# Performance work log

Hardware: AMD Instinct MI355X
Metric: run time of the kernel (lower is better)

The kernel has to match this reference:

```python
import jax, jax.numpy as jnp
import numpy as np

DIM = 1024
NUM_HEADS = 16
HEAD_DIM = DIM // NUM_HEADS
SCALE = HEAD_DIM ** -0.5


def setup_inputs() -> dict:
    key = jax.random.key(0)
    ks = jax.random.split(key, 6)
    B, N, C = 2, 2048, DIM
    std = C ** -0.5
    return {
        "x_t": jax.random.normal(ks[0], (B, N, C), dtype=jnp.float32),
        "x_s": jax.random.normal(ks[1], (B, N, C), dtype=jnp.float32),
        "W_q": jax.random.normal(ks[2], (C, C), dtype=jnp.float32) * std,
        "W_kv": jax.random.normal(ks[3], (C, 2 * C), dtype=jnp.float32) * std,
        "W_fuse": jax.random.normal(ks[4], (C, C), dtype=jnp.float32) * std,
        "b_fuse": jax.random.normal(ks[5], (C,), dtype=jnp.float32) * 0.01,
    }


def reference(x_t, x_s, W_q, W_kv, W_fuse, b_fuse):
    B, N, C = x_t.shape
    H, D = NUM_HEADS, HEAD_DIM
    # q projection (no bias, qkv_bias=False): [B,N,C] -> [B,H,N,D]
    q = (x_t @ W_q).reshape(B, N, H, D).transpose(0, 2, 1, 3)
    # kv projection: [B,N,2C] -> k,v each [B,H,N,D]
    kv = (x_s @ W_kv).reshape(B, N, 2, H, D).transpose(2, 0, 3, 1, 4)
    k, v = kv[0], kv[1]
    # attention scores [B,H,N,N]
    attn = jnp.einsum("bhnd,bhmd->bhnm", q, k) * SCALE
    attn = jax.nn.softmax(attn, axis=-1)
    # weighted values -> [B,N,C]
    a = jnp.einsum("bhnm,bhmd->bhnd", attn, v).transpose(0, 2, 1, 3).reshape(B, N, C)
    # fuse projection (with bias); dropouts are identity (p=0)
    return a @ W_fuse + b_fuse
```

## Files before the change

kernel.cpp:

```cpp
#include <hip/hip_runtime.h>

#define SEQ 2048

typedef short short8 __attribute__((ext_vector_type(8)));
typedef float floatx4 __attribute__((ext_vector_type(4)));
typedef unsigned int uint2v __attribute__((ext_vector_type(2)));
typedef unsigned int uint4v __attribute__((ext_vector_type(4)));
typedef __fp16 f16x8 __attribute__((ext_vector_type(8)));

static __device__ __forceinline__ unsigned short f2bf(float f) {
    unsigned int u = __builtin_bit_cast(unsigned int, f);
    u = (u + 0x7fffu + ((u >> 16) & 1u)) >> 16;
    return (unsigned short)u;
}

#if __has_builtin(__builtin_amdgcn_cvt_pk_bf16_f32)
typedef __bf16 bf16x2 __attribute__((ext_vector_type(2)));
static __device__ __forceinline__ unsigned int pk_bf16(float a, float b) {
    bf16x2 v = __builtin_amdgcn_cvt_pk_bf16_f32(a, b);
    return __builtin_bit_cast(unsigned int, v);
}
#else
static __device__ __forceinline__ unsigned int pk_bf16(float a, float b) {
    return (unsigned int)f2bf(a) | ((unsigned int)f2bf(b) << 16);
}
#endif

static __device__ __forceinline__ unsigned int pk_f16(float a, float b) {
    auto v = __builtin_amdgcn_cvt_pkrtz(a, b);
    return __builtin_bit_cast(unsigned int, v);
}

#define GLD16(gp, lp)                                                        \
    __builtin_amdgcn_global_load_lds(                                        \
        (const __attribute__((address_space(1))) unsigned int*)(gp),         \
        (__attribute__((address_space(3))) unsigned int*)(lp), 16, 0, 0)

__global__ void prep_kernel(const float4* __restrict__ xa, const float4* __restrict__ xb,
                            ushort4* __restrict__ oa, ushort4* __restrict__ ob, float sa,
                            const float* __restrict__ Wq, const float* __restrict__ Wkv,
                            const float* __restrict__ Wf,
                            unsigned short* __restrict__ oq, unsigned short* __restrict__ okv,
                            unsigned short* __restrict__ of_) {
    __shared__ float tile[32][33];
    int bx = blockIdx.x, tid = threadIdx.x;
    if (bx < 8192) {
        int i = bx * 256 + tid;
        if (i < 1048576) {
            float4 v = xa[i];
            ushort4 o;
            o.x = f2bf(v.x * sa); o.y = f2bf(v.y * sa);
            o.z = f2bf(v.z * sa); o.w = f2bf(v.w * sa);
            oa[i] = o;
        } else {
            int j = i - 1048576;
            float4 v = xb[j];
            ushort4 o;
            o.x = f2bf(v.x); o.y = f2bf(v.y);
            o.z = f2bf(v.z); o.w = f2bf(v.w);
            ob[j] = o;
        }
        return;
    }
    int t2 = bx - 8192;
    const float* in; unsigned short* out; int N, t;
    if (t2 < 1024)      { in = Wq;  out = oq;  N = 1024; t = t2; }
    else if (t2 < 3072) { in = Wkv; out = okv; N = 2048; t = t2 - 1024; }
    else                { in = Wf;  out = of_; N = 1024; t = t2 - 3072; }
    int nb = N >> 5;
    int n0 = (t % nb) * 32, k0 = (t / nb) * 32;
    int tx = tid & 31, ty = tid >> 5;
#pragma unroll
    for (int i = 0; i < 4; i++)
        tile[ty + i * 8][tx] = in[(size_t)(k0 + ty + i * 8) * N + n0 + tx];
    __syncthreads();
#pragma unroll
    for (int i = 0; i < 4; i++)
        out[(size_t)(n0 + ty + i * 8) * 1024 + k0 + tx] = f2bf(tile[tx][ty + i * 8]);
}

__global__ __launch_bounds__(256, 3)
void gemm_qkv(const unsigned short* __restrict__ xt,
              const unsigned short* __restrict__ xs,
              const unsigned short* __restrict__ wq,
              const unsigned short* __restrict__ wkv,
              unsigned short* __restrict__ q_ws,
              unsigned short* __restrict__ k_ws,
              unsigned short* __restrict__ vt_ws) {
    __shared__ __align__(16) unsigned short smem_[16384];
    auto sA = (unsigned short(*)[64])smem_;
    auto sB = (unsigned short(*)[64])(smem_ + 8192);
    int tid = threadIdx.x, wave = tid >> 6, lane = tid & 63;
    int l15 = lane & 15, quad = lane >> 4;
    int cx = blockIdx.x;
    bool isq = cx < 8, isv = cx >= 16;
    const unsigned short* A  = isq ? xt : xs;
    const unsigned short* Bt = isq ? wq : wkv;
    int C0 = (isq ? cx : cx - 8) * 128;
    int R0 = blockIdx.y * 128;
    int wr = (wave >> 1) * 64, wc = (wave & 1) * 64;
    int srow = lane >> 3, scol = (lane & 7) * 8;

    floatx4 acc[4][4];
#pragma unroll
    for (int i = 0; i < 4; i++)
#pragma unroll
        for (int j = 0; j < 4; j++) acc[i][j] = (floatx4){0.f, 0.f, 0.f, 0.f};

    for (int kt = 0; kt < 16; kt++) {
        __syncthreads();
#pragma unroll
        for (int c = 0; c < 4; c++) {
            int rb = wave * 32 + c * 8;
            GLD16(&A [(size_t)(R0 + rb + srow) * 1024 + kt * 64 + scol], &sA[rb][0]);
            GLD16(&Bt[(size_t)(C0 + rb + srow) * 1024 + kt * 64 + scol], &sB[rb][0]);
        }
        __syncthreads();
#pragma unroll
        for (int ks = 0; ks < 2; ks++) {
            short8 af[4], bf[4];
#pragma unroll
            for (int mt = 0; mt < 4; mt++)
                af[mt] = *(const short8*)&sA[wr + mt * 16 + l15][ks * 32 + quad * 8];
#pragma unroll
            for (int nt = 0; nt < 4; nt++)
                bf[nt] = *(const short8*)&sB[wc + nt * 16 + l15][ks * 32 + quad * 8];
#pragma unroll
            for (int mt = 0; mt < 4; mt++)
#pragma unroll
                for (int nt = 0; nt < 4; nt++)
                    acc[mt][nt] = __builtin_amdgcn_mfma_f32_16x16x32_bf16(af[mt], bf[nt], acc[mt][nt], 0, 0, 0);
        }
    }

    int b = R0 >> 11, n0 = R0 & 2047;
    __syncthreads();

    if (!isv) {
#pragma unroll
        for (int mt = 0; mt < 4; mt++)
#pragma unroll
            for (int nt = 0; nt < 4; nt++) {
                int col = wc + nt * 16 + l15;
#pragma unroll
                for (int r = 0; r < 4; r++)
                    smem_[(wr + mt * 16 + quad * 4 + r) * 128 + col] = f2bf(acc[mt][nt][r]);
            }
        __syncthreads();
        unsigned short* out = isq ? q_ws : k_ws;
#pragma unroll
        for (int i = 0; i < 8; i++) {
            int u = tid + i * 256;
            int row = u >> 4, colg = u & 15;
            int n = n0 + row;
            int gc = C0 + colg * 8;
            int h = gc >> 6, d0 = gc & 63;
            int dd = isq ? d0 : ((((d0 >> 3) ^ (n & 7)) << 3));
            *(uint4v*)&out[((size_t)((b * 16 + h) * 2048 + n)) * 64 + dd] =
                *(const uint4v*)&smem_[row * 128 + colg * 8];
        }
    } else {
#pragma unroll
        for (int mt = 0; mt < 4; mt++)
#pragma unroll
            for (int nt = 0; nt < 4; nt++) {
                int cc = wc + nt * 16 + l15;
                int nl4 = (wr + mt * 16 + quad * 4) >> 2;
                int sw = nl4 ^ ((cc & 3) << 1);
                uint2v pk;
                pk.x = pk_f16(acc[mt][nt][0], acc[mt][nt][1]);
                pk.y = pk_f16(acc[mt][nt][2], acc[mt][nt][3]);
                *(uint2v*)&smem_[cc * 128 + (sw << 2)] = pk;
            }
        __syncthreads();
        int cb = C0 - 1024;
#pragma unroll
        for (int i = 0; i < 8; i++) {
            int u = tid + i * 256;
            int cc = u >> 4, ng = u & 15;
            int sw0 = (2 * ng) ^ ((cc & 3) << 1);
            uint4v val = *(const uint4v*)&smem_[cc * 128 + (sw0 << 2)];
            int ccv = cb + cc, h = ccv >> 6, d = ccv & 63;
            *(uint4v*)&vt_ws[((size_t)((b * 16 + h) * 64 + d)) * 2048 + n0 + ng * 8] = val;
        }
    }
}

__global__ __launch_bounds__(256, 3)
void gemm_fuse(const unsigned short* __restrict__ A,
               const unsigned short* __restrict__ Bt,
               float* __restrict__ out, const float* __restrict__ bias) {
    __shared__ unsigned short sA[128][64];
    __shared__ unsigned short sB[64][64];
    int tid = threadIdx.x, wave = tid >> 6, lane = tid & 63;
    int l15 = lane & 15, quad = lane >> 4;
    int R0 = blockIdx.y * 128, C0 = blockIdx.x * 64;
    int wr = (wave >> 1) * 64, wc = (wave & 1) * 32;
    int srow = lane >> 3, scol = (lane & 7) * 8;

    floatx4 acc[4][2];
#pragma unroll
    for (int i = 0; i < 4; i++)
#pragma unroll
        for (int j = 0; j < 2; j++) acc[i][j] = (floatx4){0.f, 0.f, 0.f, 0.f};

    for (int kt = 0; kt < 16; kt++) {
        __syncthreads();
#pragma unroll
        for (int c = 0; c < 4; c++) {
            int rb = wave * 32 + c * 8;
            GLD16(&A[(size_t)(R0 + rb + srow) * 1024 + kt * 64 + scol], &sA[rb][0]);
        }
#pragma unroll
        for (int c = 0; c < 2; c++) {
            int rb = wave * 16 + c * 8;
            GLD16(&Bt[(size_t)(C0 + rb + srow) * 1024 + kt * 64 + scol], &sB[rb][0]);
        }
        __syncthreads();
#pragma unroll
        for (int ks = 0; ks < 2; ks++) {
            short8 af[4], bf[2];
#pragma unroll
            for (int mt = 0; mt < 4; mt++)
                af[mt] = *(const short8*)&sA[wr + mt * 16 + l15][ks * 32 + quad * 8];
#pragma unroll
            for (int nt = 0; nt < 2; nt++)
                bf[nt] = *(const short8*)&sB[wc + nt * 16 + l15][ks * 32 + quad * 8];
#pragma unroll
            for (int mt = 0; mt < 4; mt++)
#pragma unroll
                for (int nt = 0; nt < 2; nt++)
                    acc[mt][nt] = __builtin_amdgcn_mfma_f32_16x16x32_bf16(af[mt], bf[nt], acc[mt][nt], 0, 0, 0);
        }
    }

#pragma unroll
    for (int mt = 0; mt < 4; mt++) {
#pragma unroll
        for (int r = 0; r < 4; r++) {
            int row = R0 + wr + mt * 16 + quad * 4 + r;
#pragma unroll
            for (int nt = 0; nt < 2; nt++) {
                int col = C0 + wc + nt * 16 + l15;
                out[(size_t)row * 1024 + col] = acc[mt][nt][r] + bias[col];
            }
        }
    }
}

__global__ __launch_bounds__(256, 2)
void attn_kernel(const unsigned short* __restrict__ Q,
                 const unsigned short* __restrict__ K,
                 const unsigned short* __restrict__ Vt,
                 unsigned short* __restrict__ Aout) {
    __shared__ __align__(16) unsigned short smem[32768];
    __shared__ float lred[4][4][16];

    int tid = threadIdx.x, wave = tid >> 6, lane = tid & 63;
    int l15 = lane & 15, quad = lane >> 4;

    int id = blockIdx.x;
    int logical = (id & 7) * 128 + (id >> 3);
    int bh = logical >> 5, qt = logical & 31;
    int b = bh >> 4, h = bh & 15;
    int qr0 = qt * 64;

    const unsigned short* Qp = Q + (size_t)bh * SEQ * 64;
    const unsigned short* Kp = K + (size_t)bh * SEQ * 64;
    const unsigned short* Vp = Vt + (size_t)bh * 64 * SEQ;

    int srow = lane >> 3, scol = (lane & 7) * 8;
    int wk0 = wave * 16;
    int vscol = scol ^ (srow << 3);

#define STAGE(t, kb)                                                          \
    {                                                                         \
        _Pragma("unroll")                                                     \
        for (int j = 0; j < 2; j++) {                                         \
            int rb = wk0 + j * 8;                                             \
            GLD16(&Kp[(size_t)((t) * 64 + rb + srow) * 64 + scol],            \
                  &smem[(kb) + rb * 64]);                                     \
            GLD16(&Vp[(size_t)(rb + srow) * 2048 + (t) * 64 + vscol],         \
                  &smem[16384 + (kb) + rb * 64]);                             \
        }                                                                     \
    }

    short8 qf[4][2];
#pragma unroll
    for (int nt = 0; nt < 4; nt++)
#pragma unroll
        for (int ks = 0; ks < 2; ks++)
            qf[nt][ks] = *(const short8*)&Qp[(size_t)(qr0 + nt * 16 + l15) * 64 + ks * 32 + quad * 8];

    STAGE(0, 0) STAGE(1, 4096) STAGE(2, 8192) STAGE(3, 12288)

    floatx4 of[4][4];
#pragma unroll
    for (int i = 0; i < 4; i++)
#pragma unroll
        for (int j = 0; j < 4; j++) of[i][j] = (floatx4){0.f, 0.f, 0.f, 0.f};
    floatx4 of_l[4];
#pragma unroll
    for (int i = 0; i < 4; i++) of_l[i] = (floatx4){0.f, 0.f, 0.f, 0.f};

    f16x8 vones;
#pragma unroll
    for (int i = 0; i < 8; i++) vones[i] = (__fp16)1.0f;

    int krow = wk0 + l15;
    int ksw = (l15 & 7) << 3;
    int kaddr0 = krow * 64 + ((quad * 8) ^ ksw);
    int kaddr1 = krow * 64 + ((32 + quad * 8) ^ ksw);
    int vcol = (wk0 + quad * 4) ^ ksw;

    asm volatile("s_waitcnt vmcnt(0)" ::: "memory");
    __syncthreads();

    auto compute_pair = [&](int kb) {
        __builtin_amdgcn_s_setprio(1);
        uint2v pka[4], pkb[4];
        {
            short8 kf0 = *(const short8*)&smem[kb + kaddr0];
            short8 kf1 = *(const short8*)&smem[kb + kaddr1];
#pragma unroll
            for (int nt = 0; nt < 4; nt++) {
                floatx4 z = (floatx4){0.f, 0.f, 0.f, 0.f};
                floatx4 s = __builtin_amdgcn_mfma_f32_16x16x32_bf16(kf0, qf[nt][0], z, 0, 0, 0);
                s = __builtin_amdgcn_mfma_f32_16x16x32_bf16(kf1, qf[nt][1], s, 0, 0, 0);
                pka[nt].x = pk_f16(__builtin_amdgcn_exp2f(s[0]), __builtin_amdgcn_exp2f(s[1]));
                pka[nt].y = pk_f16(__builtin_amdgcn_exp2f(s[2]), __builtin_amdgcn_exp2f(s[3]));
            }
        }
        {
            short8 kf0 = *(const short8*)&smem[kb + 4096 + kaddr0];
            short8 kf1 = *(const short8*)&smem[kb + 4096 + kaddr1];
#pragma unroll
            for (int nt = 0; nt < 4; nt++) {
                floatx4 z = (floatx4){0.f, 0.f, 0.f, 0.f};
                floatx4 s = __builtin_amdgcn_mfma_f32_16x16x32_bf16(kf0, qf[nt][0], z, 0, 0, 0);
                s = __builtin_amdgcn_mfma_f32_16x16x32_bf16(kf1, qf[nt][1], s, 0, 0, 0);
                pkb[nt].x = pk_f16(__builtin_amdgcn_exp2f(s[0]), __builtin_amdgcn_exp2f(s[1]));
                pkb[nt].y = pk_f16(__builtin_amdgcn_exp2f(s[2]), __builtin_amdgcn_exp2f(s[3]));
            }
        }
#pragma unroll
        for (int dt = 0; dt < 4; dt++) {
            int vbase = 16384 + kb + (dt * 16 + l15) * 64 + vcol;
            uint2v va = *(const uint2v*)&smem[vbase];
            uint2v vb = *(const uint2v*)&smem[vbase + 4096];
            f16x8 vf = __builtin_bit_cast(f16x8, (uint4v){va.x, va.y, vb.x, vb.y});
#pragma unroll
            for (int nt = 0; nt < 4; nt++) {
                f16x8 pf = __builtin_bit_cast(f16x8, (uint4v){pka[nt].x, pka[nt].y, pkb[nt].x, pkb[nt].y});
                of[dt][nt] = __builtin_amdgcn_mfma_f32_16x16x32_f16(vf, pf, of[dt][nt], 0, 0, 0);
            }
        }
#pragma unroll
        for (int nt = 0; nt < 4; nt++) {
            f16x8 pf = __builtin_bit_cast(f16x8, (uint4v){pka[nt].x, pka[nt].y, pkb[nt].x, pkb[nt].y});
            of_l[nt] = __builtin_amdgcn_mfma_f32_16x16x32_f16(vones, pf, of_l[nt], 0, 0, 0);
        }
        __builtin_amdgcn_s_setprio(0);
    };

#pragma unroll 2
    for (int p = 0; p < 14; p++) {
        int kb = (p & 1) * 8192;
        compute_pair(kb);
        __builtin_amdgcn_sched_barrier(0);
        asm volatile("s_barrier" ::: "memory");
        STAGE(2 * p + 4, kb)
        STAGE(2 * p + 5, kb + 4096)
        asm volatile("s_waitcnt vmcnt(8)" ::: "memory");
        asm volatile("s_barrier" ::: "memory");
        __builtin_amdgcn_sched_barrier(0);
    }
    compute_pair(0);
    asm volatile("s_waitcnt vmcnt(0)" ::: "memory");
    asm volatile("s_barrier" ::: "memory");
    compute_pair(8192);
#undef STAGE

    if (quad == 0) {
#pragma unroll
        for (int nt = 0; nt < 4; nt++) lred[wave][nt][l15] = of_l[nt][0];
    }
    __syncthreads();

    float* red = (float*)smem;

#define RED_WRITE(C, DTC)                                                          \
    _Pragma("unroll")                                                              \
    for (int nt = 0; nt < 4; nt++)                                                 \
        *(floatx4*)&red[((C) * 4 + wave) * 1024 + nt * 256 + lane * 4] = of[DTC][nt];

#define RED_STORE(DT, C, W0, W1, W2)                                               \
    {                                                                              \
        size_t obase = (size_t)(b * SEQ + qr0) * 1024 + h * 64 + (DT) * 16 + quad * 4; \
        _Pragma("unroll")                                                          \
        for (int nt = 0; nt < 4; nt++) {                                           \
            floatx4 a0 = *(const floatx4*)&red[((C) * 4 + (W0)) * 1024 + nt * 256 + lane * 4]; \
            floatx4 a1 = *(const floatx4*)&red[((C) * 4 + (W1)) * 1024 + nt * 256 + lane * 4]; \
            floatx4 a2 = *(const floatx4*)&red[((C) * 4 + (W2)) * 1024 + nt * 256 + lane * 4]; \
            floatx4 s = of[DT][nt] + a0 + a1 + a2;                                 \
            float lt = lred[0][nt][l15] + lred[1][nt][l15] + lred[2][nt][l15] + lred[3][nt][l15]; \
            float inv = 1.f / lt;                                                  \
            uint2v o;                                                              \
            o.x = pk_bf16(s[0] * inv, s[1] * inv);                                 \
            o.y = pk_bf16(s[2] * inv, s[3] * inv);                                 \
            *(uint2v*)&Aout[obase + (size_t)(nt * 16 + l15) * 1024] = o;           \
        }                                                                          \
    }

    RED_WRITE(0, 0)
    RED_WRITE(1, 1)
    __syncthreads();
    if (wave == 0)      RED_STORE(0, 0, 1, 2, 3)
    else if (wave == 1) RED_STORE(1, 1, 0, 2, 3)
    __syncthreads();
    RED_WRITE(0, 2)
    RED_WRITE(1, 3)
    __syncthreads();
    if (wave == 2)      RED_STORE(2, 0, 0, 1, 3)
    else if (wave == 3) RED_STORE(3, 1, 0, 1, 2)
#undef RED_WRITE
#undef RED_STORE
}

extern "C" void kernel_launch(void* const* d_in, const int* in_sizes, int n_in,
                              void* d_out, int out_size, void* d_ws, size_t ws_size,
                              hipStream_t stream) {
    const float* x_t  = (const float*)d_in[0];
    const float* x_s  = (const float*)d_in[1];
    const float* W_q  = (const float*)d_in[2];
    const float* W_kv = (const float*)d_in[3];
    const float* W_f  = (const float*)d_in[4];
    const float* b_f  = (const float*)d_in[5];
    float* out = (float*)d_out;

    char* ws = (char*)d_ws;
    const size_t MB = 1u << 20;
    unsigned short* xt_bf = (unsigned short*)(ws);
    unsigned short* xs_bf = (unsigned short*)(ws + 8 * MB);
    unsigned short* wq_t  = (unsigned short*)(ws + 16 * MB);
    unsigned short* wkv_t = (unsigned short*)(ws + 18 * MB);
    unsigned short* wf_t  = (unsigned short*)(ws + 22 * MB);
    unsigned short* q_ws  = (unsigned short*)(ws + 24 * MB);
    unsigned short* k_ws  = (unsigned short*)(ws + 32 * MB);
    unsigned short* vt_ws = (unsigned short*)(ws + 40 * MB);
    unsigned short* a_ws  = (unsigned short*)(ws + 48 * MB);

    prep_kernel<<<12288, 256, 0, stream>>>((const float4*)x_t, (const float4*)x_s,
                                           (ushort4*)xt_bf, (ushort4*)xs_bf,
                                           0.125f * 1.44269504088896340736f,
                                           W_q, W_kv, W_f, wq_t, wkv_t, wf_t);

    gemm_qkv<<<dim3(24, 32), 256, 0, stream>>>(xt_bf, xs_bf, wq_t, wkv_t, q_ws, k_ws, vt_ws);
    attn_kernel<<<1024, 256, 0, stream>>>(q_ws, k_ws, vt_ws, a_ws);
    gemm_fuse<<<dim3(16, 32), 256, 0, stream>>>(a_ws, wf_t, out, b_f);
}
```

Measured before the change: 199.5 us.

## Split attention block into two query-row groups of four waves

The attention kernel now launches 512 threads per block instead of 256. The eight waves split into two groups of four, each handling 32 query rows while sharing the staged K/V tiles, and each wave issues half the global loads per stage. The point is more waves in flight to hide latency and less per-wave register pressure, since the accumulators halve. The cost is a larger 8-wave reduction through shared memory, and launch_bounds(512,4) asks for higher occupancy, which LDS use (about 64KB per block) may not allow.

```diff
diff --git a/kernel.cpp b/kernel.cpp
--- a/kernel.cpp
+++ b/kernel.cpp
@@ -248,60 +248,58 @@
     }
 }
 
-__global__ __launch_bounds__(256, 2)
+__global__ __launch_bounds__(512, 4)
 void attn_kernel(const unsigned short* __restrict__ Q,
                  const unsigned short* __restrict__ K,
                  const unsigned short* __restrict__ Vt,
                  unsigned short* __restrict__ Aout) {
     __shared__ __align__(16) unsigned short smem[32768];
-    __shared__ float lred[4][4][16];
+    __shared__ float lred[8][2][16];
 
     int tid = threadIdx.x, wave = tid >> 6, lane = tid & 63;
     int l15 = lane & 15, quad = lane >> 4;
+    int kq = wave & 3;
+    int g  = wave >> 2;
 
     int id = blockIdx.x;
     int logical = (id & 7) * 128 + (id >> 3);
     int bh = logical >> 5, qt = logical & 31;
     int b = bh >> 4, h = bh & 15;
-    int qr0 = qt * 64;
+    int qr0 = qt * 64 + g * 32;
 
     const unsigned short* Qp = Q + (size_t)bh * SEQ * 64;
     const unsigned short* Kp = K + (size_t)bh * SEQ * 64;
     const unsigned short* Vp = Vt + (size_t)bh * 64 * SEQ;
 
     int srow = lane >> 3, scol = (lane & 7) * 8;
-    int wk0 = wave * 16;
     int vscol = scol ^ (srow << 3);
+    int wk0 = kq * 16;
 
 #define STAGE(t, kb)                                                          \
     {                                                                         \
-        _Pragma("unroll")                                                     \
-        for (int j = 0; j < 2; j++) {                                         \
-            int rb = wk0 + j * 8;                                             \
-            GLD16(&Kp[(size_t)((t) * 64 + rb + srow) * 64 + scol],            \
-                  &smem[(kb) + rb * 64]);                                     \
-            GLD16(&Vp[(size_t)(rb + srow) * 2048 + (t) * 64 + vscol],         \
-                  &smem[16384 + (kb) + rb * 64]);                             \
-        }                                                                     \
-    }
-
-    short8 qf[4][2];
-#pragma unroll
-    for (int nt = 0; nt < 4; nt++)
+        GLD16(&Kp[(size_t)((t) * 64 + wave * 8 + srow) * 64 + scol],          \
+              &smem[(kb) + wave * 8 * 64]);                                   \
+        GLD16(&Vp[(size_t)(wave * 8 + srow) * 2048 + (t) * 64 + vscol],       \
+              &smem[16384 + (kb) + wave * 8 * 64]);                           \
+    }
+
+    short8 qf[2][2];
+#pragma unroll
+    for (int nt = 0; nt < 2; nt++)
 #pragma unroll
         for (int ks = 0; ks < 2; ks++)
             qf[nt][ks] = *(const short8*)&Qp[(size_t)(qr0 + nt * 16 + l15) * 64 + ks * 32 + quad * 8];
 
     STAGE(0, 0) STAGE(1, 4096) STAGE(2, 8192) STAGE(3, 12288)
 
-    floatx4 of[4][4];
+    floatx4 of[4][2];
 #pragma unroll
     for (int i = 0; i < 4; i++)
 #pragma unroll
-        for (int j = 0; j < 4; j++) of[i][j] = (floatx4){0.f, 0.f, 0.f, 0.f};
-    floatx4 of_l[4];
-#pragma unroll
-    for (int i = 0; i < 4; i++) of_l[i] = (floatx4){0.f, 0.f, 0.f, 0.f};
+        for (int j = 0; j < 2; j++) of[i][j] = (floatx4){0.f, 0.f, 0.f, 0.f};
+    floatx4 of_l[2];
+#pragma unroll
+    for (int i = 0; i < 2; i++) of_l[i] = (floatx4){0.f, 0.f, 0.f, 0.f};
 
     f16x8 vones;
 #pragma unroll
@@ -318,12 +316,12 @@
 
     auto compute_pair = [&](int kb) {
         __builtin_amdgcn_s_setprio(1);
-        uint2v pka[4], pkb[4];
+        uint2v pka[2], pkb[2];
         {
             short8 kf0 = *(const short8*)&smem[kb + kaddr0];
             short8 kf1 = *(const short8*)&smem[kb + kaddr1];
 #pragma unroll
-            for (int nt = 0; nt < 4; nt++) {
+            for (int nt = 0; nt < 2; nt++) {
                 floatx4 z = (floatx4){0.f, 0.f, 0.f, 0.f};
                 floatx4 s = __builtin_amdgcn_mfma_f32_16x16x32_bf16(kf0, qf[nt][0], z, 0, 0, 0);
                 s = __builtin_amdgcn_mfma_f32_16x16x32_bf16(kf1, qf[nt][1], s, 0, 0, 0);
@@ -335,7 +333,7 @@
             short8 kf0 = *(const short8*)&smem[kb + 4096 + kaddr0];
             short8 kf1 = *(const short8*)&smem[kb + 4096 + kaddr1];
 #pragma unroll
-            for (int nt = 0; nt < 4; nt++) {
+            for (int nt = 0; nt < 2; nt++) {
                 floatx4 z = (floatx4){0.f, 0.f, 0.f, 0.f};
                 floatx4 s = __builtin_amdgcn_mfma_f32_16x16x32_bf16(kf0, qf[nt][0], z, 0, 0, 0);
                 s = __builtin_amdgcn_mfma_f32_16x16x32_bf16(kf1, qf[nt][1], s, 0, 0, 0);
@@ -350,13 +348,13 @@
             uint2v vb = *(const uint2v*)&smem[vbase + 4096];
             f16x8 vf = __builtin_bit_cast(f16x8, (uint4v){va.x, va.y, vb.x, vb.y});
 #pragma unroll
-            for (int nt = 0; nt < 4; nt++) {
+            for (int nt = 0; nt < 2; nt++) {
                 f16x8 pf = __builtin_bit_cast(f16x8, (uint4v){pka[nt].x, pka[nt].y, pkb[nt].x, pkb[nt].y});
                 of[dt][nt] = __builtin_amdgcn_mfma_f32_16x16x32_f16(vf, pf, of[dt][nt], 0, 0, 0);
             }
         }
 #pragma unroll
-        for (int nt = 0; nt < 4; nt++) {
+        for (int nt = 0; nt < 2; nt++) {
             f16x8 pf = __builtin_bit_cast(f16x8, (uint4v){pka[nt].x, pka[nt].y, pkb[nt].x, pkb[nt].y});
             of_l[nt] = __builtin_amdgcn_mfma_f32_16x16x32_f16(vones, pf, of_l[nt], 0, 0, 0);
         }
@@ -371,7 +369,7 @@
         asm volatile("s_barrier" ::: "memory");
         STAGE(2 * p + 4, kb)
         STAGE(2 * p + 5, kb + 4096)
-        asm volatile("s_waitcnt vmcnt(8)" ::: "memory");
+        asm volatile("s_waitcnt vmcnt(4)" ::: "memory");
         asm volatile("s_barrier" ::: "memory");
         __builtin_amdgcn_sched_barrier(0);
     }
@@ -383,48 +381,37 @@
 
     if (quad == 0) {
 #pragma unroll
-        for (int nt = 0; nt < 4; nt++) lred[wave][nt][l15] = of_l[nt][0];
+        for (int nt = 0; nt < 2; nt++) lred[wave][nt][l15] = of_l[nt][0];
     }
     __syncthreads();
 
     float* red = (float*)smem;
 
-#define RED_WRITE(C, DTC)                                                          \
-    _Pragma("unroll")                                                              \
-    for (int nt = 0; nt < 4; nt++)                                                 \
-        *(floatx4*)&red[((C) * 4 + wave) * 1024 + nt * 256 + lane * 4] = of[DTC][nt];
-
-#define RED_STORE(DT, C, W0, W1, W2)                                               \
-    {                                                                              \
-        size_t obase = (size_t)(b * SEQ + qr0) * 1024 + h * 64 + (DT) * 16 + quad * 4; \
-        _Pragma("unroll")                                                          \
-        for (int nt = 0; nt < 4; nt++) {                                           \
-            floatx4 a0 = *(const floatx4*)&red[((C) * 4 + (W0)) * 1024 + nt * 256 + lane * 4]; \
-            floatx4 a1 = *(const floatx4*)&red[((C) * 4 + (W1)) * 1024 + nt * 256 + lane * 4]; \
-            floatx4 a2 = *(const floatx4*)&red[((C) * 4 + (W2)) * 1024 + nt * 256 + lane * 4]; \
-            floatx4 s = of[DT][nt] + a0 + a1 + a2;                                 \
-            float lt = lred[0][nt][l15] + lred[1][nt][l15] + lred[2][nt][l15] + lred[3][nt][l15]; \
-            float inv = 1.f / lt;                                                  \
-            uint2v o;                                                              \
-            o.x = pk_bf16(s[0] * inv, s[1] * inv);                                 \
-            o.y = pk_bf16(s[2] * inv, s[3] * inv);                                 \
-            *(uint2v*)&Aout[obase + (size_t)(nt * 16 + l15) * 1024] = o;           \
-        }                                                                          \
-    }
-
-    RED_WRITE(0, 0)
-    RED_WRITE(1, 1)
+#pragma unroll
+    for (int dt = 0; dt < 4; dt++)
+#pragma unroll
+        for (int nt = 0; nt < 2; nt++)
+            *(floatx4*)&red[(wave * 8 + dt * 2 + nt) * 256 + lane * 4] = of[dt][nt];
     __syncthreads();
-    if (wave == 0)      RED_STORE(0, 0, 1, 2, 3)
-    else if (wave == 1) RED_STORE(1, 1, 0, 2, 3)
-    __syncthreads();
-    RED_WRITE(0, 2)
-    RED_WRITE(1, 3)
-    __syncthreads();
-    if (wave == 2)      RED_STORE(2, 0, 0, 1, 3)
-    else if (wave == 3) RED_STORE(3, 1, 0, 1, 2)
-#undef RED_WRITE
-#undef RED_STORE
+
+    {
+        int mydt = kq;
+#pragma unroll
+        for (int nt = 0; nt < 2; nt++) {
+            floatx4 s = *(const floatx4*)&red[((g * 4 + 0) * 8 + mydt * 2 + nt) * 256 + lane * 4];
+#pragma unroll
+            for (int wg = 1; wg < 4; wg++)
+                s += *(const floatx4*)&red[((g * 4 + wg) * 8 + mydt * 2 + nt) * 256 + lane * 4];
+            float lt = lred[g * 4 + 0][nt][l15] + lred[g * 4 + 1][nt][l15] +
+                       lred[g * 4 + 2][nt][l15] + lred[g * 4 + 3][nt][l15];
+            float inv = 1.f / lt;
+            int row = qr0 + nt * 16 + l15;
+            uint2v o;
+            o.x = pk_bf16(s[0] * inv, s[1] * inv);
+            o.y = pk_bf16(s[2] * inv, s[3] * inv);
+            *(uint2v*)&Aout[(size_t)(b * SEQ + row) * 1024 + h * 64 + mydt * 16 + quad * 4] = o;
+        }
+    }
 }
 
 extern "C" void kernel_launch(void* const* d_in, const int* in_sizes, int n_in,
@@ -456,6 +443,6 @@
                                            W_q, W_kv, W_f, wq_t, wkv_t, wf_t);
 
     gemm_qkv<<<dim3(24, 32), 256, 0, stream>>>(xt_bf, xs_bf, wq_t, wkv_t, q_ws, k_ws, vt_ws);
-    attn_kernel<<<1024, 256, 0, stream>>>(q_ws, k_ws, vt_ws, a_ws);
+    attn_kernel<<<1024, 512, 0, stream>>>(q_ws, k_ws, vt_ws, a_ws);
     gemm_fuse<<<dim3(16, 32), 256, 0, stream>>>(a_ws, wf_t, out, b_f);
 }
```

Result: faster. 195.3 us (-2.1%).
